# Kernel tuning notes

Hardware: AMD Instinct MI355X
Metric: run time of the kernel (lower is better)

The kernel has to match this reference:

```python
import jax, jax.numpy as jnp
import numpy as np

N, E, B = 10000, 160000, 4096
DIN, H, C, HID, HEU = 768, 4, 256, 256, 6

def _gelu(x):
    return jax.nn.gelu(x, approximate=False)

def setup_inputs() -> dict:
    key = jax.random.key(0)
    ks = jax.random.split(key, 30)
    s = 0.02
    inp = {
        'semantic_embeddings': jax.random.normal(ks[0], (B, 2 * DIN), jnp.float32),
        'graph_x': jax.random.normal(ks[1], (N, DIN), jnp.float32),
        'graph_edge_index': jax.random.randint(ks[2], (2, E), 0, N, dtype=jnp.int32),
        'graph_edge_weight': jax.random.uniform(ks[3], (E, 1), jnp.float32),
        'heuristic_features': jax.random.uniform(ks[4], (B, HEU), jnp.float32),
        'node_indices': jax.random.randint(ks[5], (B,), 0, N, dtype=jnp.int32),
        # semantic_proj: Linear(1536,256) GELU Linear(256,256)
        'sem_w1': jax.random.normal(ks[6], (HID, 2 * DIN)) * s,
        'sem_b1': jnp.zeros((HID,), jnp.float32),
        'sem_w2': jax.random.normal(ks[7], (HID, HID)) * s,
        'sem_b2': jnp.zeros((HID,), jnp.float32),
        # GATConv(768 -> 256, heads=4, concat, edge_dim=1)
        'lin_w': jax.random.normal(ks[8], (H * C, DIN)) * s,
        'lin_edge_w': jax.random.normal(ks[9], (H * C, 1)) * s,
        'att_src': jax.random.normal(ks[10], (1, H, C)) * s,
        'att_dst': jax.random.normal(ks[11], (1, H, C)) * s,
        'att_edge': jax.random.normal(ks[12], (1, H, C)) * s,
        'gat_bias': jnp.zeros((H * C,), jnp.float32),
        # structural_proj: Linear(1024,256) GELU
        'struct_w': jax.random.normal(ks[13], (HID, H * C)) * s,
        'struct_b': jnp.zeros((HID,), jnp.float32),
        # HierarchicalResidualFusion
        'gate_w': jax.random.normal(ks[14], (HID, 2 * HID)) * s,
        'gate_b': jnp.zeros((HID,), jnp.float32),
        'heur_w': jax.random.normal(ks[15], (HID, HEU)) * s,
        'heur_b': jnp.zeros((HID,), jnp.float32),
        'hw': jnp.asarray(0.7, jnp.float32),
        'sw1': jax.random.normal(ks[16], (HID, HID)) * s,
        'sb1': jnp.zeros((HID,), jnp.float32),
        'sw2': jax.random.normal(ks[17], (1, HID)) * s,
        'sb2': jnp.zeros((1,), jnp.float32),
    }
    return inp

def reference(semantic_embeddings, graph_x, graph_edge_index, graph_edge_weight,
              heuristic_features, node_indices,
              sem_w1, sem_b1, sem_w2, sem_b2,
              lin_w, lin_edge_w, att_src, att_dst, att_edge, gat_bias,
              struct_w, struct_b,
              gate_w, gate_b, heur_w, heur_b, hw, sw1, sb1, sw2, sb2):
    # --- semantic projection (dropout = identity at eval) ---
    h = _gelu(semantic_embeddings @ sem_w1.T + sem_b1)
    h_sem = h @ sem_w2.T + sem_b2  # [B, HID]

    # --- GATConv with edge_dim=1, add_self_loops (edge_attr fill = mean) ---
    Nn = graph_x.shape[0]
    src = jnp.concatenate([graph_edge_index[0], jnp.arange(Nn, dtype=graph_edge_index.dtype)])
    dst = jnp.concatenate([graph_edge_index[1], jnp.arange(Nn, dtype=graph_edge_index.dtype)])
    ea = jnp.concatenate([graph_edge_weight,
                          jnp.broadcast_to(graph_edge_weight.mean(0, keepdims=True), (Nn, 1))], axis=0)
    x_proj = (graph_x @ lin_w.T).reshape(Nn, H, C)          # [N,H,C]
    a_src_n = (x_proj * att_src).sum(-1)                     # [N,H]
    a_dst_n = (x_proj * att_dst).sum(-1)                     # [N,H]
    e_proj = (ea @ lin_edge_w.T).reshape(-1, H, C)           # [E+N,H,C]
    alpha = a_src_n[src] + a_dst_n[dst] + (e_proj * att_edge).sum(-1)  # [E+N,H]
    alpha = jax.nn.leaky_relu(alpha, 0.2)
    amax = jax.ops.segment_max(alpha, dst, num_segments=Nn)
    expa = jnp.exp(alpha - amax[dst])
    denom = jax.ops.segment_sum(expa, dst, num_segments=Nn)
    coef = expa / denom[dst]                                 # softmax per dst node/head
    msg = x_proj[src] * coef[:, :, None]                     # [E+N,H,C]
    out = jax.ops.segment_sum(msg, dst, num_segments=Nn).reshape(Nn, H * C) + gat_bias
    h_graph = jax.nn.elu(out)

    # --- structural projection on selected nodes ---
    h_struct = _gelu(h_graph[node_indices] @ struct_w.T + struct_b)  # [B,HID]

    # --- hierarchical residual fusion ---
    h_heur = _gelu(heuristic_features @ heur_w.T + heur_b)
    g = jax.nn.sigmoid(jnp.concatenate([h_sem, h_struct], axis=-1) @ gate_w.T + gate_b)
    h_learned = g * h_sem + (1.0 - g) * h_struct
    h_fused = hw * h_heur + (1.0 - hw) * h_learned
    scores = (_gelu(h_fused @ sw1.T + sb1) @ sw2.T + sb2).squeeze(-1)  # [B]
    return scores
```

## Files before the change

kernel.cpp:

```cpp
#include <hip/hip_runtime.h>
#include <math.h>

#define DEV __device__ __forceinline__

typedef __attribute__((ext_vector_type(8))) short bf16x8;
typedef __attribute__((ext_vector_type(4))) float f32x4;

DEV float gelu_f(float x) { return 0.5f * x * (1.f + erff(x * 0.70710678118654752440f)); }

DEV unsigned short f2bf(float f) {
    unsigned u = __float_as_uint(f);
    u += 0x7FFF + ((u >> 16) & 1);
    return (unsigned short)(u >> 16);
}
DEV float bf2f(unsigned short h) { return __uint_as_float(((unsigned)h) << 16); }
DEV void split2(float v, unsigned short& h, unsigned short& l) {
    h = f2bf(v);
    l = f2bf(v - bf2f(h));
}

DEV void gload_lds16(const void* g, void* l) {
    __builtin_amdgcn_global_load_lds((const __attribute__((address_space(1))) void*)g,
                                     (__attribute__((address_space(3))) void*)l, 16, 0, 0);
}

template<int FM, int FN, int WR, int WC, int EPI, int GATHER, int ASRC, int OUT, int SPLIT>
DEV void gemm_body(char* ldsbase, int swz,
                   const unsigned short* __restrict__ Ah, const unsigned short* __restrict__ Al,
                   const float* __restrict__ Af, const int* __restrict__ gidx,
                   const unsigned short* __restrict__ Wh, const unsigned short* __restrict__ Wl,
                   const float* __restrict__ bias,
                   float* __restrict__ C, unsigned short* __restrict__ Ch,
                   int ldsp, int coff,
                   const float* __restrict__ fs_hsem, const float* __restrict__ fs_hstruct,
                   const float* __restrict__ fs_heur, const float* __restrict__ fs_heurw,
                   const float* __restrict__ fs_heurb, const float* __restrict__ fs_hw,
                   int M, int N, int K, int nbx)
{
    constexpr int BK = 64;
    constexpr int BM = WR * FM * 16, BN = WC * FN * 16;
    constexpr int NW = WR * WC;
    char* p = ldsbase;
    unsigned short* sAh = (unsigned short*)p; p += BM * BK * 2;
    unsigned short* sAl = nullptr;
    if constexpr (SPLIT) { sAl = (unsigned short*)p; p += BM * BK * 2; }
    unsigned short* sWh = (unsigned short*)p; p += BN * BK * 2;
    unsigned short* sWl = nullptr;
    if constexpr (SPLIT) { sWl = (unsigned short*)p; }

    const int tid = threadIdx.x;
    const int lane = tid & 63;
    const int wid = tid >> 6;
    const int wr = wid / WC, wc = wid % WC;

    const int bx = swz % nbx, by = swz / nbx;
    const int row0 = by * BM;
    const int col0 = bx * BN;

    f32x4 acc[FM][FN];
#pragma unroll
    for (int i = 0; i < FM; i++)
#pragma unroll
        for (int j = 0; j < FN; j++) acc[i][j] = (f32x4){0.f, 0.f, 0.f, 0.f};

    const int srow = lane >> 3;
    const int sslot = lane & 7;

    for (int k0 = 0; k0 < K; k0 += BK) {
#pragma unroll
        for (int c = 0; c < BM / 8 / NW; c++) {
            int call = c * NW + wid;
            int r = call * 8 + srow;
            int gr = row0 + r;
            gr = gr < M ? gr : M - 1;
            if (ASRC == 0) {
                if (GATHER) gr = gidx[gr];
                int b = (sslot ^ (r & 7)) << 4;
                gload_lds16((const char*)(Ah + (size_t)gr * K + k0) + b, (char*)sAh + call * 1024);
                if (SPLIT)
                    gload_lds16((const char*)(Al + (size_t)gr * K + k0) + b, (char*)sAl + call * 1024);
            } else {
                const float* sp = Af + (size_t)gr * K + k0 + sslot * 8;
                float vv[8];
                *(float4*)&vv[0] = *(const float4*)sp;
                *(float4*)&vv[4] = *(const float4*)(sp + 4);
                union { bf16x8 v; unsigned short u[8]; } ph, pl;
#pragma unroll
                for (int q = 0; q < 8; q++) {
                    if (SPLIT) split2(vv[q], ph.u[q], pl.u[q]);
                    else       ph.u[q] = f2bf(vv[q]);
                }
                int b = (sslot ^ (r & 7)) << 4;
                *(bf16x8*)((char*)sAh + r * 128 + b) = ph.v;
                if (SPLIT) *(bf16x8*)((char*)sAl + r * 128 + b) = pl.v;
            }
        }
#pragma unroll
        for (int c = 0; c < BN / 8 / NW; c++) {
            int call = c * NW + wid;
            int r = call * 8 + srow;
            int gr = col0 + r;
            int b = (sslot ^ (r & 7)) << 4;
            gload_lds16((const char*)(Wh + (size_t)gr * K + k0) + b, (char*)sWh + call * 1024);
            if (SPLIT)
                gload_lds16((const char*)(Wl + (size_t)gr * K + k0) + b, (char*)sWl + call * 1024);
        }
        __syncthreads();

        const int fr = lane & 15, kq = lane >> 4;
#pragma unroll
        for (int ks = 0; ks < 2; ks++) {
            bf16x8 ah[FM], al[FM], bh[FN], bl[FN];
#pragma unroll
            for (int i = 0; i < FM; i++) {
                int r = wr * FM * 16 + i * 16 + fr;
                int b = ((ks * 4 + kq) ^ (r & 7)) << 4;
                ah[i] = *(const bf16x8*)((const char*)sAh + r * 128 + b);
                if (SPLIT) al[i] = *(const bf16x8*)((const char*)sAl + r * 128 + b);
            }
#pragma unroll
            for (int j = 0; j < FN; j++) {
                int r = wc * FN * 16 + j * 16 + fr;
                int b = ((ks * 4 + kq) ^ (r & 7)) << 4;
                bh[j] = *(const bf16x8*)((const char*)sWh + r * 128 + b);
                if (SPLIT) bl[j] = *(const bf16x8*)((const char*)sWl + r * 128 + b);
            }
#pragma unroll
            for (int i = 0; i < FM; i++)
#pragma unroll
                for (int j = 0; j < FN; j++) {
                    acc[i][j] = __builtin_amdgcn_mfma_f32_16x16x32_bf16(ah[i], bh[j], acc[i][j], 0, 0, 0);
                    if (SPLIT) {
                        acc[i][j] = __builtin_amdgcn_mfma_f32_16x16x32_bf16(al[i], bh[j], acc[i][j], 0, 0, 0);
                        acc[i][j] = __builtin_amdgcn_mfma_f32_16x16x32_bf16(ah[i], bl[j], acc[i][j], 0, 0, 0);
                    }
                }
        }
        __syncthreads();
    }

    const int fr = lane & 15;
    const int r0 = (lane >> 4) * 4;
#pragma unroll
    for (int i = 0; i < FM; i++) {
#pragma unroll
        for (int jj = 0; jj < 4; jj++) {
            int gr = row0 + wr * FM * 16 + i * 16 + r0 + jj;
            if (gr >= M) continue;
            float sacc = 0.f;
#pragma unroll
            for (int j = 0; j < FN; j++) {
                int gc = col0 + wc * FN * 16 + j * 16 + fr;
                float v = acc[i][j][jj] + (bias ? bias[gc] : 0.f);
                if (EPI == 1) v = gelu_f(v);
                else if (EPI == 3) {
                    float g = 1.f / (1.f + expf(-v));
                    float hh = fs_heurb[gc];
#pragma unroll
                    for (int q = 0; q < 6; q++) hh = fmaf(fs_heur[gr * 6 + q], fs_heurw[gc * 6 + q], hh);
                    hh = gelu_f(hh);
                    float hl = g * fs_hsem[(size_t)gr * 256 + gc] + (1.f - g) * fs_hstruct[(size_t)gr * 256 + gc];
                    float hwv = fs_hw[0];
                    v = hwv * hh + (1.f - hwv) * hl;
                }
                if (OUT == 0 || OUT == 2) C[(size_t)gr * N + gc] = v;
                if (OUT == 2 || OUT == 3) Ch[(size_t)gr * ldsp + coff + gc] = f2bf(v);
                if (OUT == 4) sacc = fmaf(v, fs_hsem[gc], sacc);
            }
            if (OUT == 4) {
                sacc += __shfl_xor(sacc, 1);
                sacc += __shfl_xor(sacc, 2);
                sacc += __shfl_xor(sacc, 4);
                sacc += __shfl_xor(sacc, 8);
                if ((lane & 15) == 0) atomicAdd(&C[gr], sacc);
            }
        }
    }
}

DEV int xcd_swz(int bid, int nwg) {
    return ((nwg & 7) == 0) ? (bid & 7) * (nwg >> 3) + (bid >> 3) : bid;
}

template<int FM, int FN, int WR, int WC, int EPI, int GATHER, int ASRC, int OUT, int SPLIT>
__global__ __launch_bounds__(WR* WC * 64)
void mgemm_k(const unsigned short* __restrict__ Ah, const unsigned short* __restrict__ Al,
             const float* __restrict__ Af, const int* __restrict__ gidx,
             const unsigned short* __restrict__ Wh, const unsigned short* __restrict__ Wl,
             const float* __restrict__ bias,
             float* __restrict__ C, unsigned short* __restrict__ Ch,
             int ldsp, int coff,
             const float* __restrict__ fs_hsem, const float* __restrict__ fs_hstruct,
             const float* __restrict__ fs_heur, const float* __restrict__ fs_heurw,
             const float* __restrict__ fs_heurb, const float* __restrict__ fs_hw,
             int M, int N, int K, int nbx)
{
    constexpr int BM = WR * FM * 16, BN = WC * FN * 16;
    constexpr int LDSB = (BM + BN) * 64 * 2 * (SPLIT ? 2 : 1);
    __shared__ alignas(16) char lds[LDSB];
    int swz = xcd_swz(blockIdx.x, gridDim.x);
    gemm_body<FM, FN, WR, WC, EPI, GATHER, ASRC, OUT, SPLIT>(
        lds, swz, Ah, Al, Af, gidx, Wh, Wl, bias, C, Ch, ldsp, coff,
        fs_hsem, fs_hstruct, fs_heur, fs_heurw, fs_heurb, fs_hw, M, N, K, nbx);
}

DEV void gat_agg_body(char* shm, int d,
                      const int* __restrict__ ei, const float* __restrict__ ew,
                      const float* __restrict__ scal, const float* __restrict__ a_src,
                      const float* __restrict__ a_dst,
                      const int* __restrict__ count, const int* __restrict__ offs_end,
                      const int* __restrict__ eid, const unsigned short* __restrict__ xpb,
                      const float* __restrict__ gat_bias,
                      unsigned short* __restrict__ aggh, unsigned short* __restrict__ aggl, int E)
{
    int* srcs   = (int*)shm;
    float* al   = (float*)(shm + 1024);
    float* mrun = (float*)(shm + 5120);
    float* drun = (float*)(shm + 5136);
    float* scale = (float*)(shm + 5152);
    int c = count[d];
    int start = offs_end[d] - c;
    int tid = threadIdx.x;
    if (tid < 4) { mrun[tid] = -1e30f; drun[tid] = 0.f; }
    float4 acc = make_float4(0.f, 0.f, 0.f, 0.f);
    const int h = tid >> 6;
    const int x = tid * 4;
    const float adst0 = a_dst[d * 4 + 0], adst1 = a_dst[d * 4 + 1],
                adst2 = a_dst[d * 4 + 2], adst3 = a_dst[d * 4 + 3];

    for (int cb = 0; cb < c; cb += 256) {
        int cc = min(256, c - cb);
        __syncthreads();
        for (int t = tid; t < cc * 4; t += 256) {
            int j = t >> 2, hh = t & 3;
            int e = eid[start + cb + j];
            int s; float ea;
            if (e < E) { s = ei[e]; ea = ew[e]; }
            else       { s = e - E; ea = scal[0] / (float)E; }
            float ad = hh == 0 ? adst0 : hh == 1 ? adst1 : hh == 2 ? adst2 : adst3;
            float a = a_src[s * 4 + hh] + ad + ea * scal[1 + hh];
            a = a > 0.f ? a : 0.2f * a;
            al[j * 4 + hh] = a;
            if (hh == 0) srcs[j] = s;
        }
        __syncthreads();
        if (tid < 4) {
            float m = -1e30f;
            for (int j = 0; j < cc; j++) m = fmaxf(m, al[j * 4 + tid]);
            float nm = fmaxf(mrun[tid], m);
            float sc = expf(mrun[tid] - nm);
            scale[tid] = sc;
            drun[tid] *= sc;
            mrun[tid] = nm;
        }
        __syncthreads();
        for (int t = tid; t < cc * 4; t += 256) {
            int j = t >> 2, hh = t & 3;
            al[j * 4 + hh] = expf(al[j * 4 + hh] - mrun[hh]);
        }
        __syncthreads();
        if (tid < 4) {
            float s = 0.f;
            for (int j = 0; j < cc; j++) s += al[j * 4 + tid];
            drun[tid] += s;
        }
        float sc = scale[h];
        acc.x *= sc; acc.y *= sc; acc.z *= sc; acc.w *= sc;
        for (int j = 0; j < cc; j++) {
            float w = al[j * 4 + h];
            ushort4 vv = *(const ushort4*)(xpb + (size_t)srcs[j] * 1024 + x);
            acc.x = fmaf(w, bf2f(vv.x), acc.x);
            acc.y = fmaf(w, bf2f(vv.y), acc.y);
            acc.z = fmaf(w, bf2f(vv.z), acc.z);
            acc.w = fmaf(w, bf2f(vv.w), acc.w);
        }
    }
    __syncthreads();
    float dn = drun[h];
    float4 gb = *(const float4*)(gat_bias + x);
    float t0 = acc.x / dn + gb.x, t1 = acc.y / dn + gb.y,
          t2 = acc.z / dn + gb.z, t3 = acc.w / dn + gb.w;
    t0 = t0 > 0.f ? t0 : expf(t0) - 1.f;
    t1 = t1 > 0.f ? t1 : expf(t1) - 1.f;
    t2 = t2 > 0.f ? t2 : expf(t2) - 1.f;
    t3 = t3 > 0.f ? t3 : expf(t3) - 1.f;
    ushort4 hh, ll;
    split2(t0, hh.x, ll.x);
    split2(t1, hh.y, ll.y);
    split2(t2, hh.z, ll.z);
    split2(t3, hh.w, ll.w);
    *(ushort4*)(aggh + (size_t)d * 1024 + x) = hh;
    *(ushort4*)(aggl + (size_t)d * 1024 + x) = ll;
}

__global__ __launch_bounds__(256)
void dualA_k(const unsigned short* __restrict__ gxh, const unsigned short* __restrict__ linw_h,
             unsigned short* __restrict__ xpb, int Nn, int HC, int DIN, int nbx_x, int nxp,
             const float* __restrict__ sem, const unsigned short* __restrict__ sw1w_h,
             const float* __restrict__ sem_b1, unsigned short* __restrict__ s1h,
             int B, int nbh, int nh1,
             const int* __restrict__ ei, int* __restrict__ offs, int* __restrict__ eid, int E)
{
    __shared__ alignas(16) char lds[32768];
    int bid = blockIdx.x;
    if (bid < nxp) {
        int swz = xcd_swz(bid, nxp);
        gemm_body<4, 4, 2, 2, 0, 0, 0, 3, 0>(
            lds, swz, gxh, nullptr, nullptr, nullptr, linw_h, nullptr, nullptr,
            nullptr, xpb, HC, 0, nullptr, nullptr, nullptr, nullptr, nullptr, nullptr,
            Nn, HC, DIN, nbx_x);
    } else if (bid < nxp + nh1) {
        int swz = xcd_swz(bid - nxp, nh1);
        gemm_body<1, 2, 2, 2, 1, 0, 1, 3, 0>(
            lds, swz, nullptr, nullptr, sem, nullptr, sw1w_h, nullptr, sem_b1,
            nullptr, s1h, 256, 0, nullptr, nullptr, nullptr, nullptr, nullptr, nullptr,
            B, 256, 2 * DIN, nbh);
    } else {
        int e = (bid - nxp - nh1) * 256 + threadIdx.x;
        if (e < E + Nn) {
            int d = (e < E) ? ei[E + e] : e - E;
            int p = atomicAdd(&offs[d], 1);
            eid[p] = e;
        }
    }
}

__global__ __launch_bounds__(256)
void dualC_k(int Nn, int nh1,
             const int* __restrict__ ei, const float* __restrict__ ew,
             const float* __restrict__ scal, const float* __restrict__ a_src,
             const float* __restrict__ a_dst, const int* __restrict__ needed,
             const int* __restrict__ count, const int* __restrict__ offs_end,
             const int* __restrict__ eid, const unsigned short* __restrict__ xpb,
             const float* __restrict__ gat_bias,
             unsigned short* __restrict__ aggh, unsigned short* __restrict__ aggl, int E,
             const unsigned short* __restrict__ s1h,
             const unsigned short* __restrict__ sw2w_h,
             const float* __restrict__ sem_b2, float* __restrict__ h_sem,
             unsigned short* __restrict__ gAh,
             int B, int nbh)
{
    __shared__ alignas(16) char lds[12288];
    int bid = blockIdx.x;
    if (bid < Nn) {
        if (!needed[bid]) return;
        gat_agg_body(lds, bid, ei, ew, scal, a_src, a_dst, count, offs_end, eid,
                     xpb, gat_bias, aggh, aggl, E);
    } else {
        int swz = xcd_swz(bid - Nn, nh1);
        gemm_body<1, 2, 2, 2, 0, 0, 0, 2, 0>(
            lds, swz, s1h, nullptr, nullptr, nullptr, sw2w_h, nullptr, sem_b2,
            h_sem, gAh, 512, 0, nullptr, nullptr, nullptr, nullptr, nullptr, nullptr,
            B, 256, 256, nbh);
    }
}


__global__ void init_k(int* count, int* needed, float* scal, int Nn,
                       const float* __restrict__ lin_w, const float* __restrict__ att_src,
                       const float* __restrict__ att_dst,
                       float* __restrict__ wsrc, float* __restrict__ wdst,
                       const float* __restrict__ lew, const float* __restrict__ ae, int ZB,
                       float* __restrict__ out, const float* __restrict__ sb2, int B,
                       int* __restrict__ cursor)
{
    int b = blockIdx.x;
    if (b < ZB) {
        int i = b * 256 + threadIdx.x;
        if (i < Nn) { count[i] = 0; needed[i] = 0; }
        if (i < B) out[i] = sb2[0];
        if (i == 0) { scal[0] = 0.f; cursor[0] = 0; }
        return;
    }
    if (b < ZB + 12) {
        int gid = (b - ZB) * 256 + threadIdx.x;
        if (gid >= 4 * 768) return;
        int h = gid / 768, k = gid % 768;
        float ss = 0.f, sd = 0.f;
        for (int c = 0; c < 256; c++) {
            float w = lin_w[(size_t)(h * 256 + c) * 768 + k];
            ss = fmaf(w, att_src[h * 256 + c], ss);
            sd = fmaf(w, att_dst[h * 256 + c], sd);
        }
        wsrc[k * 4 + h] = ss;
        wdst[k * 4 + h] = sd;
        return;
    }
    int w = threadIdx.x / 64, lane = threadIdx.x % 64;
    float c = 0.f;
    for (int cc = lane; cc < 256; cc += 64) c += lew[w * 256 + cc] * ae[w * 256 + cc];
    for (int off = 32; off; off >>= 1) c += __shfl_down(c, off);
    if (lane == 0) scal[1 + w] = c;
}

__global__ __launch_bounds__(256)
void mega1_k(int Nn, int nW, int nCnt, int nMark, int nEw,
             const float* __restrict__ gx, unsigned short* __restrict__ gxh,
             const float* __restrict__ wsrc, const float* __restrict__ wdst,
             float* __restrict__ a_src, float* __restrict__ a_dst,
             const float* s0, unsigned short* h0, unsigned short* l0, int e0,
             const float* s1, unsigned short* h1, unsigned short* l1, int e1,
             const float* s2, unsigned short* h2, unsigned short* l2, int e2,
             const float* s3, unsigned short* h3, unsigned short* l3, int e3,
             const float* s4, unsigned short* h4, unsigned short* l4, int e4,
             const float* s5, unsigned short* h5, unsigned short* l5, int e5,
             const int* __restrict__ ei, int* __restrict__ count, int E,
             const int* __restrict__ nidx, int* __restrict__ needed, int B,
             const float* __restrict__ ew, float* __restrict__ scal)
{
    __shared__ float sh[256];
    int b = blockIdx.x;
    int t = threadIdx.x;

    if (b < Nn) {
        int node = b;
        float acc[8] = {0.f, 0.f, 0.f, 0.f, 0.f, 0.f, 0.f, 0.f};
        if (t < 192) {
            float4 v = ((const float4*)(gx + (size_t)node * 768))[t];
            ushort4 h;
            h.x = f2bf(v.x); h.y = f2bf(v.y); h.z = f2bf(v.z); h.w = f2bf(v.w);
            ((ushort4*)(gxh + (size_t)node * 768))[t] = h;
            float vv[4] = {v.x, v.y, v.z, v.w};
#pragma unroll
            for (int q = 0; q < 4; q++) {
                int k = t * 4 + q;
                float4 wsv = *(const float4*)(wsrc + k * 4);
                float4 wdv = *(const float4*)(wdst + k * 4);
                acc[0] = fmaf(vv[q], wsv.x, acc[0]); acc[1] = fmaf(vv[q], wsv.y, acc[1]);
                acc[2] = fmaf(vv[q], wsv.z, acc[2]); acc[3] = fmaf(vv[q], wsv.w, acc[3]);
                acc[4] = fmaf(vv[q], wdv.x, acc[4]); acc[5] = fmaf(vv[q], wdv.y, acc[5]);
                acc[6] = fmaf(vv[q], wdv.z, acc[6]); acc[7] = fmaf(vv[q], wdv.w, acc[7]);
            }
        }
#pragma unroll
        for (int i = 0; i < 8; i++)
            for (int off = 32; off; off >>= 1) acc[i] += __shfl_down(acc[i], off);
        int lane = t & 63, wid = t >> 6;
        if (lane == 0)
#pragma unroll
            for (int i = 0; i < 8; i++) sh[wid * 8 + i] = acc[i];
        __syncthreads();
        if (t < 8) {
            float s = sh[t] + sh[8 + t] + sh[16 + t] + sh[24 + t];
            if (t < 4) a_src[node * 4 + t] = s;
            else       a_dst[node * 4 + (t - 4)] = s;
        }
        return;
    }
    b -= Nn;
    if (b < nW) {
        int i = b * 256 + t;
        const float* s; unsigned short* h; unsigned short* l; int j;
        if (i < e0)      { s = s0; h = h0; l = l0; j = i; }
        else if (i < e1) { s = s1; h = h1; l = l1; j = i - e0; }
        else if (i < e2) { s = s2; h = h2; l = l2; j = i - e1; }
        else if (i < e3) { s = s3; h = h3; l = l3; j = i - e2; }
        else if (i < e4) { s = s4; h = h4; l = l4; j = i - e3; }
        else if (i < e5) { s = s5; h = h5; l = l5; j = i - e4; }
        else return;
        float4 v = ((const float4*)s)[j];
        ushort4 hh, ll;
        split2(v.x, hh.x, ll.x);
        split2(v.y, hh.y, ll.y);
        split2(v.z, hh.z, ll.z);
        split2(v.w, hh.w, ll.w);
        ((ushort4*)h)[j] = hh;
        ((ushort4*)l)[j] = ll;
        return;
    }
    b -= nW;
    if (b < nCnt) {
        int e = b * 256 + t;
        if (e >= E + Nn) return;
        int d = (e < E) ? ei[E + e] : e - E;
        atomicAdd(&count[d], 1);
        return;
    }
    b -= nCnt;
    if (b < nMark) {
        int gid = b * 256 + t;
        if (gid < B) needed[nidx[gid]] = 1;
        return;
    }
    b -= nMark;
    float s = 0.f;
    for (int i = b * 256 + t; i < E; i += nEw * 256) s += ew[i];
    sh[t] = s;
    __syncthreads();
    for (int off = 128; off; off >>= 1) {
        if (t < off) sh[t] += sh[t + off];
        __syncthreads();
    }
    if (t == 0) atomicAdd(&scal[0], sh[0]);
}

__global__ void alloc_k(const int* __restrict__ count, int* __restrict__ offs,
                        int* __restrict__ cursor, int Nn)
{
    int d = blockIdx.x * 256 + threadIdx.x;
    if (d < Nn) offs[d] = atomicAdd(cursor, count[d]);
}


extern "C" void kernel_launch(void* const* d_in, const int* in_sizes, int n_in,
                              void* d_out, int out_size, void* d_ws, size_t ws_size,
                              hipStream_t stream)
{
    const float* sem      = (const float*)d_in[0];
    const float* gx       = (const float*)d_in[1];
    const int*   ei       = (const int*)d_in[2];
    const float* ew       = (const float*)d_in[3];
    const float* heur     = (const float*)d_in[4];
    const int*   nidx     = (const int*)d_in[5];
    const float* sem_w1   = (const float*)d_in[6];
    const float* sem_b1   = (const float*)d_in[7];
    const float* sem_w2   = (const float*)d_in[8];
    const float* sem_b2   = (const float*)d_in[9];
    const float* lin_w    = (const float*)d_in[10];
    const float* lin_edge = (const float*)d_in[11];
    const float* att_src  = (const float*)d_in[12];
    const float* att_dst  = (const float*)d_in[13];
    const float* att_edge = (const float*)d_in[14];
    const float* gat_bias = (const float*)d_in[15];
    const float* struct_w = (const float*)d_in[16];
    const float* struct_b = (const float*)d_in[17];
    const float* gate_w   = (const float*)d_in[18];
    const float* gate_b   = (const float*)d_in[19];
    const float* heur_w   = (const float*)d_in[20];
    const float* heur_b   = (const float*)d_in[21];
    const float* hwp      = (const float*)d_in[22];
    const float* sw1      = (const float*)d_in[23];
    const float* sb1      = (const float*)d_in[24];
    const float* sw2      = (const float*)d_in[25];
    const float* sb2      = (const float*)d_in[26];
    float* out = (float*)d_out;

    const int DIN = 768, HC = 1024, HID = 256;
    const int B  = in_sizes[0] / (2 * DIN);
    const int Nn = in_sizes[1] / DIN;
    const int E  = in_sizes[3];

    float* ws = (float*)d_ws;
    size_t off = 0;
    auto alloc = [&](size_t n) { float* p = ws + off; off += n; return p; };
    auto allocU = [&](size_t nelem) { return (unsigned short*)alloc((nelem + 1) / 2); };

    unsigned short* xpb  = allocU((size_t)Nn * HC);
    unsigned short* aggh = allocU((size_t)Nn * HC);
    unsigned short* aggl = allocU((size_t)Nn * HC);
    float* h_sem    = alloc((size_t)B * HID);
    float* h_struct = alloc((size_t)B * HID);
    unsigned short* s1h = allocU((size_t)B * HID);
    unsigned short* gAh = allocU((size_t)B * 512);
    unsigned short* fuh = allocU((size_t)B * HID);
    float* a_src    = alloc((size_t)Nn * 4);
    float* a_dst    = alloc((size_t)Nn * 4);
    float* wsrc     = alloc((size_t)DIN * 4);
    float* wdst     = alloc((size_t)DIN * 4);
    int* countb     = (int*)alloc((size_t)Nn);
    int* offsb      = (int*)alloc((size_t)Nn);
    int* neededb    = (int*)alloc((size_t)Nn);
    int* eidb       = (int*)alloc((size_t)(E + Nn));
    float* scal     = alloc(8);
    int* cursorb    = (int*)alloc(4);
    unsigned short* linw_h = allocU((size_t)HC * DIN);
    unsigned short* linw_l = allocU((size_t)HC * DIN);
    unsigned short* sw1w_h = allocU((size_t)HID * 2 * DIN);
    unsigned short* sw1w_l = allocU((size_t)HID * 2 * DIN);
    unsigned short* sw2w_h = allocU((size_t)HID * HID);
    unsigned short* sw2w_l = allocU((size_t)HID * HID);
    unsigned short* stw_h  = allocU((size_t)HID * HC);
    unsigned short* stw_l  = allocU((size_t)HID * HC);
    unsigned short* gaw_h  = allocU((size_t)HID * 512);
    unsigned short* gaw_l  = allocU((size_t)HID * 512);
    unsigned short* scw_h  = allocU((size_t)HID * HID);
    unsigned short* scw_l  = allocU((size_t)HID * HID);
    unsigned short* gxh    = allocU((size_t)Nn * DIN);
    (void)ws_size; (void)n_in; (void)out_size;

    int ZB = (Nn + 255) / 256;
    init_k<<<ZB + 13, 256, 0, stream>>>(countb, neededb, scal, Nn,
                                        lin_w, att_src, att_dst, wsrc, wdst,
                                        lin_edge, att_edge, ZB, out, sb2, B, cursorb);

    int c0 = (HC * DIN) / 4;
    int c1 = c0 + (HID * 2 * DIN) / 4;
    int c2 = c1 + (HID * HID) / 4;
    int c3 = c2 + (HID * HC) / 4;
    int c4 = c3 + (HID * 512) / 4;
    int c5 = c4 + (HID * HID) / 4;
    int nW = (c5 + 255) / 256;
    int tot = E + Nn;
    int nCnt = (tot + 255) / 256;
    int nMark = (B + 255) / 256;
    int nEw = 256;
    mega1_k<<<Nn + nW + nCnt + nMark + nEw, 256, 0, stream>>>(
        Nn, nW, nCnt, nMark, nEw,
        gx, gxh, wsrc, wdst, a_src, a_dst,
        lin_w, linw_h, linw_l, c0,
        sem_w1, sw1w_h, sw1w_l, c1,
        sem_w2, sw2w_h, sw2w_l, c2,
        struct_w, stw_h, stw_l, c3,
        gate_w, gaw_h, gaw_l, c4,
        sw1, scw_h, scw_l, c5,
        ei, countb, E,
        nidx, neededb, B,
        ew, scal);

    alloc_k<<<(Nn + 255) / 256, 256, 0, stream>>>(countb, offsb, cursorb, Nn);

    const int nbx_x = HC / 128;
    const int nby_x = (Nn + 127) / 128;
    const int nxp = nbx_x * nby_x;
    const int nbh = HID / 64;
    const int nh1 = (B / 32) * nbh;
    const int nF = (tot + 255) / 256;
    dualA_k<<<nxp + nh1 + nF, 256, 0, stream>>>(gxh, linw_h, xpb, Nn, HC, DIN, nbx_x, nxp,
                                                sem, sw1w_h, sem_b1, s1h,
                                                B, nbh, nh1, ei, offsb, eidb, E);

    dualC_k<<<Nn + nh1, 256, 0, stream>>>(Nn, nh1,
                                          ei, ew, scal, a_src, a_dst, neededb, countb, offsb, eidb,
                                          xpb, gat_bias, aggh, aggl, E,
                                          s1h, sw2w_h, sem_b2, h_sem, gAh, B, nbh);

    mgemm_k<1, 2, 2, 2, 1, 1, 0, 2, 1><<<nh1, 256, 0, stream>>>(
        aggh, aggl, nullptr, nidx, stw_h, stw_l, struct_b,
        h_struct, gAh, 512, 256, nullptr, nullptr, nullptr, nullptr, nullptr, nullptr,
        B, HID, HC, nbh);

    mgemm_k<1, 2, 2, 2, 3, 0, 0, 3, 0><<<nh1, 256, 0, stream>>>(
        gAh, nullptr, nullptr, nullptr, gaw_h, nullptr, gate_b,
        nullptr, fuh, HID, 0, h_sem, h_struct, heur, heur_w, heur_b, hwp,
        B, HID, 512, nbh);

    mgemm_k<1, 2, 2, 2, 1, 0, 0, 4, 0><<<nh1, 256, 0, stream>>>(
        fuh, nullptr, nullptr, nullptr, scw_h, nullptr, sb1,
        out, nullptr, 0, 0, sw2, nullptr, nullptr, nullptr, nullptr, nullptr,
        B, HID, HID, nbh);
}
```

Baseline: 184.8 us.

## Drop split-bf16 precision path and fuse gate and score GEMMs into one tail kernel

Result: no change. 187.7 us (+1.6%).

```diff
diff --git a/kernel.cpp b/kernel.cpp
--- a/kernel.cpp
+++ b/kernel.cpp
@@ -14,39 +14,25 @@
     return (unsigned short)(u >> 16);
 }
 DEV float bf2f(unsigned short h) { return __uint_as_float(((unsigned)h) << 16); }
-DEV void split2(float v, unsigned short& h, unsigned short& l) {
-    h = f2bf(v);
-    l = f2bf(v - bf2f(h));
-}
 
 DEV void gload_lds16(const void* g, void* l) {
     __builtin_amdgcn_global_load_lds((const __attribute__((address_space(1))) void*)g,
                                      (__attribute__((address_space(3))) void*)l, 16, 0, 0);
 }
 
-template<int FM, int FN, int WR, int WC, int EPI, int GATHER, int ASRC, int OUT, int SPLIT>
+template<int FM, int FN, int WR, int WC, int EPI, int GATHER, int ASRC, int OUT>
 DEV void gemm_body(char* ldsbase, int swz,
-                   const unsigned short* __restrict__ Ah, const unsigned short* __restrict__ Al,
-                   const float* __restrict__ Af, const int* __restrict__ gidx,
-                   const unsigned short* __restrict__ Wh, const unsigned short* __restrict__ Wl,
-                   const float* __restrict__ bias,
+                   const unsigned short* __restrict__ Ah, const float* __restrict__ Af,
+                   const int* __restrict__ gidx,
+                   const unsigned short* __restrict__ Wh, const float* __restrict__ bias,
                    float* __restrict__ C, unsigned short* __restrict__ Ch,
-                   int ldsp, int coff,
-                   const float* __restrict__ fs_hsem, const float* __restrict__ fs_hstruct,
-                   const float* __restrict__ fs_heur, const float* __restrict__ fs_heurw,
-                   const float* __restrict__ fs_heurb, const float* __restrict__ fs_hw,
-                   int M, int N, int K, int nbx)
+                   int ldsp, int coff, int M, int N, int K, int nbx)
 {
     constexpr int BK = 64;
     constexpr int BM = WR * FM * 16, BN = WC * FN * 16;
     constexpr int NW = WR * WC;
-    char* p = ldsbase;
-    unsigned short* sAh = (unsigned short*)p; p += BM * BK * 2;
-    unsigned short* sAl = nullptr;
-    if constexpr (SPLIT) { sAl = (unsigned short*)p; p += BM * BK * 2; }
-    unsigned short* sWh = (unsigned short*)p; p += BN * BK * 2;
-    unsigned short* sWl = nullptr;
-    if constexpr (SPLIT) { sWl = (unsigned short*)p; }
+    unsigned short* sAh = (unsigned short*)ldsbase;
+    unsigned short* sWh = (unsigned short*)(ldsbase + BM * BK * 2);
 
     const int tid = threadIdx.x;
     const int lane = tid & 63;
@@ -77,22 +63,16 @@
                 if (GATHER) gr = gidx[gr];
                 int b = (sslot ^ (r & 7)) << 4;
                 gload_lds16((const char*)(Ah + (size_t)gr * K + k0) + b, (char*)sAh + call * 1024);
-                if (SPLIT)
-                    gload_lds16((const char*)(Al + (size_t)gr * K + k0) + b, (char*)sAl + call * 1024);
             } else {
                 const float* sp = Af + (size_t)gr * K + k0 + sslot * 8;
                 float vv[8];
                 *(float4*)&vv[0] = *(const float4*)sp;
                 *(float4*)&vv[4] = *(const float4*)(sp + 4);
-                union { bf16x8 v; unsigned short u[8]; } ph, pl;
-#pragma unroll
-                for (int q = 0; q < 8; q++) {
-                    if (SPLIT) split2(vv[q], ph.u[q], pl.u[q]);
-                    else       ph.u[q] = f2bf(vv[q]);
-                }
+                union { bf16x8 v; unsigned short u[8]; } ph;
+#pragma unroll
+                for (int q = 0; q < 8; q++) ph.u[q] = f2bf(vv[q]);
                 int b = (sslot ^ (r & 7)) << 4;
                 *(bf16x8*)((char*)sAh + r * 128 + b) = ph.v;
-                if (SPLIT) *(bf16x8*)((char*)sAl + r * 128 + b) = pl.v;
             }
         }
 #pragma unroll
@@ -102,39 +82,30 @@
             int gr = col0 + r;
             int b = (sslot ^ (r & 7)) << 4;
             gload_lds16((const char*)(Wh + (size_t)gr * K + k0) + b, (char*)sWh + call * 1024);
-            if (SPLIT)
-                gload_lds16((const char*)(Wl + (size_t)gr * K + k0) + b, (char*)sWl + call * 1024);
         }
         __syncthreads();
 
         const int fr = lane & 15, kq = lane >> 4;
 #pragma unroll
         for (int ks = 0; ks < 2; ks++) {
-            bf16x8 ah[FM], al[FM], bh[FN], bl[FN];
+            bf16x8 ah[FM], bh[FN];
 #pragma unroll
             for (int i = 0; i < FM; i++) {
                 int r = wr * FM * 16 + i * 16 + fr;
                 int b = ((ks * 4 + kq) ^ (r & 7)) << 4;
                 ah[i] = *(const bf16x8*)((const char*)sAh + r * 128 + b);
-                if (SPLIT) al[i] = *(const bf16x8*)((const char*)sAl + r * 128 + b);
             }
 #pragma unroll
             for (int j = 0; j < FN; j++) {
                 int r = wc * FN * 16 + j * 16 + fr;
                 int b = ((ks * 4 + kq) ^ (r & 7)) << 4;
                 bh[j] = *(const bf16x8*)((const char*)sWh + r * 128 + b);
-                if (SPLIT) bl[j] = *(const bf16x8*)((const char*)sWl + r * 128 + b);
             }
 #pragma unroll
             for (int i = 0; i < FM; i++)
 #pragma unroll
-                for (int j = 0; j < FN; j++) {
+                for (int j = 0; j < FN; j++)
                     acc[i][j] = __builtin_amdgcn_mfma_f32_16x16x32_bf16(ah[i], bh[j], acc[i][j], 0, 0, 0);
-                    if (SPLIT) {
-                        acc[i][j] = __builtin_amdgcn_mfma_f32_16x16x32_bf16(al[i], bh[j], acc[i][j], 0, 0, 0);
-                        acc[i][j] = __builtin_amdgcn_mfma_f32_16x16x32_bf16(ah[i], bl[j], acc[i][j], 0, 0, 0);
-                    }
-                }
         }
         __syncthreads();
     }
@@ -147,32 +118,13 @@
         for (int jj = 0; jj < 4; jj++) {
             int gr = row0 + wr * FM * 16 + i * 16 + r0 + jj;
             if (gr >= M) continue;
-            float sacc = 0.f;
 #pragma unroll
             for (int j = 0; j < FN; j++) {
                 int gc = col0 + wc * FN * 16 + j * 16 + fr;
                 float v = acc[i][j][jj] + (bias ? bias[gc] : 0.f);
                 if (EPI == 1) v = gelu_f(v);
-                else if (EPI == 3) {
-                    float g = 1.f / (1.f + expf(-v));
-                    float hh = fs_heurb[gc];
-#pragma unroll
-                    for (int q = 0; q < 6; q++) hh = fmaf(fs_heur[gr * 6 + q], fs_heurw[gc * 6 + q], hh);
-                    hh = gelu_f(hh);
-                    float hl = g * fs_hsem[(size_t)gr * 256 + gc] + (1.f - g) * fs_hstruct[(size_t)gr * 256 + gc];
-                    float hwv = fs_hw[0];
-                    v = hwv * hh + (1.f - hwv) * hl;
-                }
                 if (OUT == 0 || OUT == 2) C[(size_t)gr * N + gc] = v;
                 if (OUT == 2 || OUT == 3) Ch[(size_t)gr * ldsp + coff + gc] = f2bf(v);
-                if (OUT == 4) sacc = fmaf(v, fs_hsem[gc], sacc);
-            }
-            if (OUT == 4) {
-                sacc += __shfl_xor(sacc, 1);
-                sacc += __shfl_xor(sacc, 2);
-                sacc += __shfl_xor(sacc, 4);
-                sacc += __shfl_xor(sacc, 8);
-                if ((lane & 15) == 0) atomicAdd(&C[gr], sacc);
             }
         }
     }
@@ -182,26 +134,168 @@
     return ((nwg & 7) == 0) ? (bid & 7) * (nwg >> 3) + (bid >> 3) : bid;
 }
 
-template<int FM, int FN, int WR, int WC, int EPI, int GATHER, int ASRC, int OUT, int SPLIT>
+template<int FM, int FN, int WR, int WC, int EPI, int GATHER, int ASRC, int OUT>
 __global__ __launch_bounds__(WR* WC * 64)
-void mgemm_k(const unsigned short* __restrict__ Ah, const unsigned short* __restrict__ Al,
-             const float* __restrict__ Af, const int* __restrict__ gidx,
-             const unsigned short* __restrict__ Wh, const unsigned short* __restrict__ Wl,
-             const float* __restrict__ bias,
+void mgemm_k(const unsigned short* __restrict__ Ah, const float* __restrict__ Af,
+             const int* __restrict__ gidx,
+             const unsigned short* __restrict__ Wh, const float* __restrict__ bias,
              float* __restrict__ C, unsigned short* __restrict__ Ch,
-             int ldsp, int coff,
-             const float* __restrict__ fs_hsem, const float* __restrict__ fs_hstruct,
-             const float* __restrict__ fs_heur, const float* __restrict__ fs_heurw,
-             const float* __restrict__ fs_heurb, const float* __restrict__ fs_hw,
-             int M, int N, int K, int nbx)
+             int ldsp, int coff, int M, int N, int K, int nbx)
 {
     constexpr int BM = WR * FM * 16, BN = WC * FN * 16;
-    constexpr int LDSB = (BM + BN) * 64 * 2 * (SPLIT ? 2 : 1);
-    __shared__ alignas(16) char lds[LDSB];
+    __shared__ alignas(16) char lds[(BM + BN) * 64 * 2];
     int swz = xcd_swz(blockIdx.x, gridDim.x);
-    gemm_body<FM, FN, WR, WC, EPI, GATHER, ASRC, OUT, SPLIT>(
-        lds, swz, Ah, Al, Af, gidx, Wh, Wl, bias, C, Ch, ldsp, coff,
-        fs_hsem, fs_hstruct, fs_heur, fs_heurw, fs_heurb, fs_hw, M, N, K, nbx);
+    gemm_body<FM, FN, WR, WC, EPI, GATHER, ASRC, OUT>(
+        lds, swz, Ah, Af, gidx, Wh, bias, C, Ch, ldsp, coff, M, N, K, nbx);
+}
+
+__global__ __launch_bounds__(256)
+void tail_k(const unsigned short* __restrict__ gAh,
+            const unsigned short* __restrict__ gaw_h,
+            const float* __restrict__ gate_b,
+            const float* __restrict__ h_sem, const float* __restrict__ h_struct,
+            const float* __restrict__ heur, const float* __restrict__ heur_w,
+            const float* __restrict__ heur_b, const float* __restrict__ hwp,
+            const unsigned short* __restrict__ scw_h,
+            const float* __restrict__ sb1, const float* __restrict__ sw2,
+            const float* __restrict__ sb2, float* __restrict__ out, int B)
+{
+    __shared__ alignas(16) char lds[36864];
+    unsigned short* sA = (unsigned short*)lds;
+    unsigned short* sW = (unsigned short*)(lds + 4096);
+    char* fu = lds + 4096;
+    float* sm = (float*)(lds + 20480);
+
+    const int tid = threadIdx.x;
+    const int lane = tid & 63;
+    const int wid = tid >> 6;
+    const int swz = xcd_swz(blockIdx.x, gridDim.x);
+    const int row0 = swz * 32;
+    const int srow = lane >> 3, sslot = lane & 7;
+    const int fr = lane & 15, kq = lane >> 4;
+
+    f32x4 acc[2][4];
+#pragma unroll
+    for (int i = 0; i < 2; i++)
+#pragma unroll
+        for (int j = 0; j < 4; j++) acc[i][j] = (f32x4){0.f, 0.f, 0.f, 0.f};
+
+    for (int k0 = 0; k0 < 512; k0 += 64) {
+        {
+            int r = wid * 8 + srow;
+            int b = (sslot ^ (r & 7)) << 4;
+            gload_lds16((const char*)(gAh + (size_t)(row0 + r) * 512 + k0) + b, (char*)sA + wid * 1024);
+        }
+#pragma unroll
+        for (int c = 0; c < 8; c++) {
+            int call = c * 4 + wid;
+            int r = call * 8 + srow;
+            int b = (sslot ^ (r & 7)) << 4;
+            gload_lds16((const char*)(gaw_h + (size_t)r * 512 + k0) + b, (char*)sW + call * 1024);
+        }
+        __syncthreads();
+#pragma unroll
+        for (int ks = 0; ks < 2; ks++) {
+            bf16x8 ah[2], bh[4];
+#pragma unroll
+            for (int i = 0; i < 2; i++) {
+                int r = i * 16 + fr;
+                int b = ((ks * 4 + kq) ^ (r & 7)) << 4;
+                ah[i] = *(const bf16x8*)((const char*)sA + r * 128 + b);
+            }
+#pragma unroll
+            for (int j = 0; j < 4; j++) {
+                int r = wid * 64 + j * 16 + fr;
+                int b = ((ks * 4 + kq) ^ (r & 7)) << 4;
+                bh[j] = *(const bf16x8*)((const char*)sW + r * 128 + b);
+            }
+#pragma unroll
+            for (int i = 0; i < 2; i++)
+#pragma unroll
+                for (int j = 0; j < 4; j++)
+                    acc[i][j] = __builtin_amdgcn_mfma_f32_16x16x32_bf16(ah[i], bh[j], acc[i][j], 0, 0, 0);
+        }
+        __syncthreads();
+    }
+
+    const int r0v = (lane >> 4) * 4;
+    const float hwv = hwp[0];
+#pragma unroll
+    for (int i = 0; i < 2; i++) {
+#pragma unroll
+        for (int jj = 0; jj < 4; jj++) {
+            int row = i * 16 + r0v + jj;
+            int gr = row0 + row;
+#pragma unroll
+            for (int j = 0; j < 4; j++) {
+                int gc = wid * 64 + j * 16 + fr;
+                float v = acc[i][j][jj] + gate_b[gc];
+                float g = 1.f / (1.f + expf(-v));
+                float hh = heur_b[gc];
+#pragma unroll
+                for (int q = 0; q < 6; q++) hh = fmaf(heur[gr * 6 + q], heur_w[gc * 6 + q], hh);
+                hh = gelu_f(hh);
+                float hl = g * h_sem[(size_t)gr * 256 + gc] + (1.f - g) * h_struct[(size_t)gr * 256 + gc];
+                v = hwv * hh + (1.f - hwv) * hl;
+                int sub = gc >> 6, slot = (gc & 63) >> 3;
+                int byteoff = row * 512 + sub * 128 + ((slot ^ (row & 7)) << 4) + (gc & 7) * 2;
+                *(unsigned short*)(fu + byteoff) = f2bf(v);
+            }
+        }
+    }
+    __syncthreads();
+
+    f32x4 acc2[2][4];
+#pragma unroll
+    for (int i = 0; i < 2; i++)
+#pragma unroll
+        for (int j = 0; j < 4; j++) acc2[i][j] = (f32x4){0.f, 0.f, 0.f, 0.f};
+
+    for (int k0 = 0; k0 < 256; k0 += 32) {
+        int sub = k0 >> 6;
+        int slotb = ((k0 & 63) >> 3) + kq;
+        bf16x8 ah2[2], bh2[4];
+#pragma unroll
+        for (int i = 0; i < 2; i++) {
+            int r = i * 16 + fr;
+            int byteoff = r * 512 + sub * 128 + ((slotb ^ (r & 7)) << 4);
+            ah2[i] = *(const bf16x8*)(fu + byteoff);
+        }
+#pragma unroll
+        for (int j = 0; j < 4; j++) {
+            int gc = wid * 64 + j * 16 + fr;
+            bh2[j] = *(const bf16x8*)(scw_h + (size_t)gc * 256 + k0 + kq * 8);
+        }
+#pragma unroll
+        for (int i = 0; i < 2; i++)
+#pragma unroll
+            for (int j = 0; j < 4; j++)
+                acc2[i][j] = __builtin_amdgcn_mfma_f32_16x16x32_bf16(ah2[i], bh2[j], acc2[i][j], 0, 0, 0);
+    }
+
+#pragma unroll
+    for (int i = 0; i < 2; i++) {
+#pragma unroll
+        for (int jj = 0; jj < 4; jj++) {
+            int row = i * 16 + r0v + jj;
+            float sacc = 0.f;
+#pragma unroll
+            for (int j = 0; j < 4; j++) {
+                int gc = wid * 64 + j * 16 + fr;
+                float v = acc2[i][j][jj] + sb1[gc];
+                v = gelu_f(v);
+                sacc = fmaf(v, sw2[gc], sacc);
+            }
+            sacc += __shfl_xor(sacc, 1);
+            sacc += __shfl_xor(sacc, 2);
+            sacc += __shfl_xor(sacc, 4);
+            sacc += __shfl_xor(sacc, 8);
+            if ((lane & 15) == 0) sm[row * 4 + wid] = sacc;
+        }
+    }
+    __syncthreads();
+    if (tid < 32)
+        out[row0 + tid] = sm[tid * 4 + 0] + sm[tid * 4 + 1] + sm[tid * 4 + 2] + sm[tid * 4 + 3] + sb2[0];
 }
 
 DEV void gat_agg_body(char* shm, int d,
@@ -211,7 +305,7 @@
                       const int* __restrict__ count, const int* __restrict__ offs_end,
                       const int* __restrict__ eid, const unsigned short* __restrict__ xpb,
                       const float* __restrict__ gat_bias,
-                      unsigned short* __restrict__ aggh, unsigned short* __restrict__ aggl, int E)
+                      unsigned short* __restrict__ aggh, int E)
 {
     int* srcs   = (int*)shm;
     float* al   = (float*)(shm + 1024);
@@ -284,13 +378,9 @@
     t1 = t1 > 0.f ? t1 : expf(t1) - 1.f;
     t2 = t2 > 0.f ? t2 : expf(t2) - 1.f;
     t3 = t3 > 0.f ? t3 : expf(t3) - 1.f;
-    ushort4 hh, ll;
-    split2(t0, hh.x, ll.x);
-    split2(t1, hh.y, ll.y);
-    split2(t2, hh.z, ll.z);
-    split2(t3, hh.w, ll.w);
+    ushort4 hh;
+    hh.x = f2bf(t0); hh.y = f2bf(t1); hh.z = f2bf(t2); hh.w = f2bf(t3);
     *(ushort4*)(aggh + (size_t)d * 1024 + x) = hh;
-    *(ushort4*)(aggl + (size_t)d * 1024 + x) = ll;
 }
 
 __global__ __launch_bounds__(256)
@@ -305,16 +395,14 @@
     int bid = blockIdx.x;
     if (bid < nxp) {
         int swz = xcd_swz(bid, nxp);
-        gemm_body<4, 4, 2, 2, 0, 0, 0, 3, 0>(
-            lds, swz, gxh, nullptr, nullptr, nullptr, linw_h, nullptr, nullptr,
-            nullptr, xpb, HC, 0, nullptr, nullptr, nullptr, nullptr, nullptr, nullptr,
-            Nn, HC, DIN, nbx_x);
+        gemm_body<4, 4, 2, 2, 0, 0, 0, 3>(
+            lds, swz, gxh, nullptr, nullptr, linw_h, nullptr,
+            nullptr, xpb, HC, 0, Nn, HC, DIN, nbx_x);
     } else if (bid < nxp + nh1) {
         int swz = xcd_swz(bid - nxp, nh1);
-        gemm_body<1, 2, 2, 2, 1, 0, 1, 3, 0>(
-            lds, swz, nullptr, nullptr, sem, nullptr, sw1w_h, nullptr, sem_b1,
-            nullptr, s1h, 256, 0, nullptr, nullptr, nullptr, nullptr, nullptr, nullptr,
-            B, 256, 2 * DIN, nbh);
+        gemm_body<1, 2, 2, 2, 1, 0, 1, 3>(
+            lds, swz, nullptr, sem, nullptr, sw1w_h, sem_b1,
+            nullptr, s1h, 256, 0, B, 256, 2 * DIN, nbh);
     } else {
         int e = (bid - nxp - nh1) * 256 + threadIdx.x;
         if (e < E + Nn) {
@@ -333,7 +421,7 @@
              const int* __restrict__ count, const int* __restrict__ offs_end,
              const int* __restrict__ eid, const unsigned short* __restrict__ xpb,
              const float* __restrict__ gat_bias,
-             unsigned short* __restrict__ aggh, unsigned short* __restrict__ aggl, int E,
+             unsigned short* __restrict__ aggh, int E,
              const unsigned short* __restrict__ s1h,
              const unsigned short* __restrict__ sw2w_h,
              const float* __restrict__ sem_b2, float* __restrict__ h_sem,
@@ -345,13 +433,12 @@
     if (bid < Nn) {
         if (!needed[bid]) return;
         gat_agg_body(lds, bid, ei, ew, scal, a_src, a_dst, count, offs_end, eid,
-                     xpb, gat_bias, aggh, aggl, E);
+                     xpb, gat_bias, aggh, E);
     } else {
         int swz = xcd_swz(bid - Nn, nh1);
-        gemm_body<1, 2, 2, 2, 0, 0, 0, 2, 0>(
-            lds, swz, s1h, nullptr, nullptr, nullptr, sw2w_h, nullptr, sem_b2,
-            h_sem, gAh, 512, 0, nullptr, nullptr, nullptr, nullptr, nullptr, nullptr,
-            B, 256, 256, nbh);
+        gemm_body<1, 2, 2, 2, 0, 0, 0, 2>(
+            lds, swz, s1h, nullptr, nullptr, sw2w_h, sem_b2,
+            h_sem, gAh, 512, 0, B, 256, 256, nbh);
     }
 }
 
@@ -361,14 +448,12 @@
                        const float* __restrict__ att_dst,
                        float* __restrict__ wsrc, float* __restrict__ wdst,
                        const float* __restrict__ lew, const float* __restrict__ ae, int ZB,
-                       float* __restrict__ out, const float* __restrict__ sb2, int B,
                        int* __restrict__ cursor)
 {
     int b = blockIdx.x;
     if (b < ZB) {
         int i = b * 256 + threadIdx.x;
         if (i < Nn) { count[i] = 0; needed[i] = 0; }
-        if (i < B) out[i] = sb2[0];
         if (i == 0) { scal[0] = 0.f; cursor[0] = 0; }
         return;
     }
@@ -398,12 +483,12 @@
              const float* __restrict__ gx, unsigned short* __restrict__ gxh,
              const float* __restrict__ wsrc, const float* __restrict__ wdst,
              float* __restrict__ a_src, float* __restrict__ a_dst,
-             const float* s0, unsigned short* h0, unsigned short* l0, int e0,
-             const float* s1, unsigned short* h1, unsigned short* l1, int e1,
-             const float* s2, unsigned short* h2, unsigned short* l2, int e2,
-             const float* s3, unsigned short* h3, unsigned short* l3, int e3,
-             const float* s4, unsigned short* h4, unsigned short* l4, int e4,
-             const float* s5, unsigned short* h5, unsigned short* l5, int e5,
+             const float* s0, unsigned short* h0, int e0,
+             const float* s1, unsigned short* h1, int e1,
+             const float* s2, unsigned short* h2, int e2,
+             const float* s3, unsigned short* h3, int e3,
+             const float* s4, unsigned short* h4, int e4,
+             const float* s5, unsigned short* h5, int e5,
              const int* __restrict__ ei, int* __restrict__ count, int E,
              const int* __restrict__ nidx, int* __restrict__ needed, int B,
              const float* __restrict__ ew, float* __restrict__ scal)
@@ -450,22 +535,18 @@
     b -= Nn;
     if (b < nW) {
         int i = b * 256 + t;
-        const float* s; unsigned short* h; unsigned short* l; int j;
-        if (i < e0)      { s = s0; h = h0; l = l0; j = i; }
-        else if (i < e1) { s = s1; h = h1; l = l1; j = i - e0; }
-        else if (i < e2) { s = s2; h = h2; l = l2; j = i - e1; }
-        else if (i < e3) { s = s3; h = h3; l = l3; j = i - e2; }
-        else if (i < e4) { s = s4; h = h4; l = l4; j = i - e3; }
-        else if (i < e5) { s = s5; h = h5; l = l5; j = i - e4; }
+        const float* s; unsigned short* h; int j;
+        if (i < e0)      { s = s0; h = h0; j = i; }
+        else if (i < e1) { s = s1; h = h1; j = i - e0; }
+        else if (i < e2) { s = s2; h = h2; j = i - e1; }
+        else if (i < e3) { s = s3; h = h3; j = i - e2; }
+        else if (i < e4) { s = s4; h = h4; j = i - e3; }
+        else if (i < e5) { s = s5; h = h5; j = i - e4; }
         else return;
         float4 v = ((const float4*)s)[j];
-        ushort4 hh, ll;
-        split2(v.x, hh.x, ll.x);
-        split2(v.y, hh.y, ll.y);
-        split2(v.z, hh.z, ll.z);
-        split2(v.w, hh.w, ll.w);
+        ushort4 hh;
+        hh.x = f2bf(v.x); hh.y = f2bf(v.y); hh.z = f2bf(v.z); hh.w = f2bf(v.w);
         ((ushort4*)h)[j] = hh;
-        ((ushort4*)l)[j] = ll;
         return;
     }
     b -= nW;
@@ -547,12 +628,10 @@
 
     unsigned short* xpb  = allocU((size_t)Nn * HC);
     unsigned short* aggh = allocU((size_t)Nn * HC);
-    unsigned short* aggl = allocU((size_t)Nn * HC);
     float* h_sem    = alloc((size_t)B * HID);
     float* h_struct = alloc((size_t)B * HID);
     unsigned short* s1h = allocU((size_t)B * HID);
     unsigned short* gAh = allocU((size_t)B * 512);
-    unsigned short* fuh = allocU((size_t)B * HID);
     float* a_src    = alloc((size_t)Nn * 4);
     float* a_dst    = alloc((size_t)Nn * 4);
     float* wsrc     = alloc((size_t)DIN * 4);
@@ -564,24 +643,18 @@
     float* scal     = alloc(8);
     int* cursorb    = (int*)alloc(4);
     unsigned short* linw_h = allocU((size_t)HC * DIN);
-    unsigned short* linw_l = allocU((size_t)HC * DIN);
     unsigned short* sw1w_h = allocU((size_t)HID * 2 * DIN);
-    unsigned short* sw1w_l = allocU((size_t)HID * 2 * DIN);
     unsigned short* sw2w_h = allocU((size_t)HID * HID);
-    unsigned short* sw2w_l = allocU((size_t)HID * HID);
     unsigned short* stw_h  = allocU((size_t)HID * HC);
-    unsigned short* stw_l  = allocU((size_t)HID * HC);
     unsigned short* gaw_h  = allocU((size_t)HID * 512);
-    unsigned short* gaw_l  = allocU((size_t)HID * 512);
     unsigned short* scw_h  = allocU((size_t)HID * HID);
-    unsigned short* scw_l  = allocU((size_t)HID * HID);
     unsigned short* gxh    = allocU((size_t)Nn * DIN);
     (void)ws_size; (void)n_in; (void)out_size;
 
     int ZB = (Nn + 255) / 256;
     init_k<<<ZB + 13, 256, 0, stream>>>(countb, neededb, scal, Nn,
                                         lin_w, att_src, att_dst, wsrc, wdst,
-                                        lin_edge, att_edge, ZB, out, sb2, B, cursorb);
+                                        lin_edge, att_edge, ZB, cursorb);
 
     int c0 = (HC * DIN) / 4;
     int c1 = c0 + (HID * 2 * DIN) / 4;
@@ -597,12 +670,12 @@
     mega1_k<<<Nn + nW + nCnt + nMark + nEw, 256, 0, stream>>>(
         Nn, nW, nCnt, nMark, nEw,
         gx, gxh, wsrc, wdst, a_src, a_dst,
-        lin_w, linw_h, linw_l, c0,
-        sem_w1, sw1w_h, sw1w_l, c1,
-        sem_w2, sw2w_h, sw2w_l, c2,
-        struct_w, stw_h, stw_l, c3,
-        gate_w, gaw_h, gaw_l, c4,
-        sw1, scw_h, scw_l, c5,
+        lin_w, linw_h, c0,
+        sem_w1, sw1w_h, c1,
+        sem_w2, sw2w_h, c2,
+        struct_w, stw_h, c3,
+        gate_w, gaw_h, c4,
+        sw1, scw_h, c5,
         ei, countb, E,
         nidx, neededb, B,
         ew, scal);
@@ -621,21 +694,14 @@
 
     dualC_k<<<Nn + nh1, 256, 0, stream>>>(Nn, nh1,
                                           ei, ew, scal, a_src, a_dst, neededb, countb, offsb, eidb,
-                                          xpb, gat_bias, aggh, aggl, E,
+                                          xpb, gat_bias, aggh, E,
                                           s1h, sw2w_h, sem_b2, h_sem, gAh, B, nbh);
 
-    mgemm_k<1, 2, 2, 2, 1, 1, 0, 2, 1><<<nh1, 256, 0, stream>>>(
-        aggh, aggl, nullptr, nidx, stw_h, stw_l, struct_b,
-        h_struct, gAh, 512, 256, nullptr, nullptr, nullptr, nullptr, nullptr, nullptr,
-        B, HID, HC, nbh);
-
-    mgemm_k<1, 2, 2, 2, 3, 0, 0, 3, 0><<<nh1, 256, 0, stream>>>(
-        gAh, nullptr, nullptr, nullptr, gaw_h, nullptr, gate_b,
-        nullptr, fuh, HID, 0, h_sem, h_struct, heur, heur_w, heur_b, hwp,
-        B, HID, 512, nbh);
-
-    mgemm_k<1, 2, 2, 2, 1, 0, 0, 4, 0><<<nh1, 256, 0, stream>>>(
-        fuh, nullptr, nullptr, nullptr, scw_h, nullptr, sb1,
-        out, nullptr, 0, 0, sw2, nullptr, nullptr, nullptr, nullptr, nullptr,
-        B, HID, HID, nbh);
-}
+    mgemm_k<1, 2, 2, 2, 1, 1, 0, 2><<<nh1, 256, 0, stream>>>(
+        aggh, nullptr, nidx, stw_h, struct_b,
+        h_struct, gAh, 512, 256, B, HID, HC, nbh);
+
+    tail_k<<<B / 32, 256, 0, stream>>>(gAh, gaw_h, gate_b, h_sem, h_struct,
+                                       heur, heur_w, heur_b, hwp,
+                                       scw_h, sb1, sw2, sb2, out, B);
+}
```
